# Optimization experiments

Hardware: AMD Instinct MI355X
Metric: run time of the kernel (lower is better)

## Reference

```python
import jax, jax.numpy as jnp
import numpy as np

D = 1024
H = 16
HD = D // H
EPS = 1e-5

def _layernorm(x, g, b):
    mu = jnp.mean(x, axis=-1, keepdims=True)
    var = jnp.mean(jnp.square(x - mu), axis=-1, keepdims=True)
    return (x - mu) * jax.lax.rsqrt(var + EPS) * g + b

def setup_inputs() -> dict:
    key = jax.random.key(0)
    ks = jax.random.split(key, 12)
    B, Sq, Skv = 8, 1024, 1024
    s = 1.0 / np.sqrt(D)  # xavier-ish scale
    return {
        "Q": jax.random.normal(ks[0], (B, Sq, D), jnp.float32),
        "K": jax.random.normal(ks[1], (B, Skv, D), jnp.float32),
        "key_padding_mask": jnp.ones((B, Skv), jnp.int32),
        "Wq": jax.random.normal(ks[2], (D, D), jnp.float32) * s,
        "bq": jnp.zeros((D,), jnp.float32),
        "Wk": jax.random.normal(ks[3], (D, D), jnp.float32) * s,
        "bk": jnp.zeros((D,), jnp.float32),
        "Wv": jax.random.normal(ks[4], (D, D), jnp.float32) * s,
        "bv": jnp.zeros((D,), jnp.float32),
        "Wp": jax.random.normal(ks[5], (D, D), jnp.float32) * s,
        "bp": jnp.zeros((D,), jnp.float32),
        "g0": jnp.ones((D,), jnp.float32),
        "beta0": jnp.zeros((D,), jnp.float32),
        "g1": jnp.ones((D,), jnp.float32),
        "beta1": jnp.zeros((D,), jnp.float32),
    }

def reference(Q, K, key_padding_mask, Wq, bq, Wk, bk, Wv, bv, Wp, bp, g0, beta0, g1, beta1):
    B, Sq, _ = Q.shape
    q = Q @ Wq + bq                      # [B,Sq,D]
    k = K @ Wk + bk                      # [B,Skv,D]
    v = K @ Wv + bv
    qh = q.reshape(B, Sq, H, HD).transpose(0, 2, 1, 3)   # [B,H,Sq,hd]
    kh = k.reshape(B, -1, H, HD).transpose(0, 2, 1, 3)   # [B,H,Skv,hd]
    vh = v.reshape(B, -1, H, HD).transpose(0, 2, 1, 3)
    attn = jnp.einsum('bhqd,bhkd->bhqk', qh, kh) / np.sqrt(HD)
    pad = (key_padding_mask == 0)[:, None, None, :]      # [B,1,1,Skv]
    attn = jnp.where(pad, -jnp.inf, attn)
    attn = jax.nn.softmax(attn, axis=-1)
    ctx = jnp.einsum('bhqk,bhkd->bhqd', attn, vh)        # [B,H,Sq,hd]
    ctx = ctx.transpose(0, 2, 1, 3).reshape(B, Sq, H * HD)
    o = _layernorm(q + ctx, g0, beta0)
    o = _layernorm(o + jax.nn.gelu(o @ Wp + bp, approximate=False), g1, beta1)
    return o
```

## Files before the change

### kernel.cpp

```cpp
#include <hip/hip_runtime.h>
#include <hip/hip_bf16.h>
#include <math.h>

#define DEV __device__ __forceinline__

typedef __bf16 bf16;
typedef __bf16 bf16x8 __attribute__((ext_vector_type(8)));
typedef __bf16 bf16x4 __attribute__((ext_vector_type(4)));
typedef float f32x4 __attribute__((ext_vector_type(4)));

static constexpr int BATCH = 8, S = 1024, D = 1024, H = 16, HD = 64;
static constexpr int M = BATCH * S;

static constexpr float QSCALE = 0.18033688f;

DEV f32x4 mfma16(bf16x8 a, bf16x8 b, f32x4 c) {
  return __builtin_amdgcn_mfma_f32_16x16x32_bf16(a, b, c, 0, 0, 0);
}

DEV void gload_lds16(const void* g, void* l) {
  __builtin_amdgcn_global_load_lds(
      (__attribute__((address_space(1))) void*)(g),
      (__attribute__((address_space(3))) void*)(l), 16, 0, 0);
}

DEV bf16x8 lds_read8(const void* base, int byteoff) {
  return *(const bf16x8*)((const char*)base + byteoff);
}


__global__ void cvt_bf16_kernel(const float* __restrict__ in0, bf16* __restrict__ out0,
                                const float* __restrict__ in1, bf16* __restrict__ out1, int n) {
  const float* in = blockIdx.y ? in1 : in0;
  bf16* out = blockIdx.y ? out1 : out0;
  int i = (blockIdx.x * blockDim.x + threadIdx.x) * 4;
  int stride = gridDim.x * blockDim.x * 4;
  for (; i < n; i += stride) {
    float4 v = *(const float4*)(in + i);
    bf16x4 o = { (bf16)v.x, (bf16)v.y, (bf16)v.z, (bf16)v.w };
    *(bf16x4*)(out + i) = o;
  }
}

__global__ void transpose_cvt_kernel(const float* __restrict__ w0, bf16* __restrict__ o0,
                                     const float* __restrict__ w1, bf16* __restrict__ o1,
                                     const float* __restrict__ w2, bf16* __restrict__ o2,
                                     const float* __restrict__ w3, bf16* __restrict__ o3) {
  const int z = blockIdx.z;
  const float* in = z == 0 ? w0 : z == 1 ? w1 : z == 2 ? w2 : w3;
  bf16* out = z == 0 ? o0 : z == 1 ? o1 : z == 2 ? o2 : o3;
  __shared__ float t[32][33];
  int n0 = blockIdx.x * 32, k0 = blockIdx.y * 32;
  int tx = threadIdx.x, ty = threadIdx.y;
  for (int i = 0; i < 32; i += 8)
    t[ty + i][tx] = in[(size_t)(k0 + ty + i) * D + n0 + tx];
  __syncthreads();
  for (int i = 0; i < 32; i += 8)
    out[(size_t)(n0 + ty + i) * D + k0 + tx] = (bf16)t[tx][ty + i];
}


struct GemmOut { float* f32; bf16* b16; float scale; };

template<int MODE>
DEV void gemm_body(const bf16* A, const bf16* Bt, const float* bias,
                   float* Cf, bf16* Cb, float osc,
                   bf16* As, bf16* Bs) {
  constexpr int K = 1024, N = 1024, BK = 32;
  const int tid = threadIdx.x, lane = tid & 63, wave = tid >> 6;
  int f = blockIdx.y * 8 + blockIdx.x;
  f = (f & 7) * 64 + (f >> 3);
  const int bm = f >> 3, bn = f & 7;
  const int wr = wave >> 1, wc = wave & 1;
  f32x4 acc[4][4] = {};
  const char* Ab = (const char*)(A + (size_t)bm * 128 * K);
  const char* Bb = (const char*)(Bt + (size_t)bn * 128 * K);

  for (int kt = 0; kt < K / BK; ++kt) {
    __syncthreads();
    const int k0b = kt * (BK * 2);
    for (int i = 0; i < 2; ++i) {
      int cbase = (wave * 2 + i) * 1024;
      int off = cbase + lane * 16;
      int row = off >> 6, col = off & 63;
      gload_lds16(Ab + (size_t)row * (K * 2) + k0b + col, (char*)As + cbase);
      gload_lds16(Bb + (size_t)row * (K * 2) + k0b + col, (char*)Bs + cbase);
    }
    __syncthreads();
    bf16x8 af[4], bfr[4];
    for (int mi = 0; mi < 4; ++mi)
      af[mi] = lds_read8(As, (wr * 64 + mi * 16 + (lane & 15)) * 64 + (lane >> 4) * 16);
    for (int ni = 0; ni < 4; ++ni)
      bfr[ni] = lds_read8(Bs, (wc * 64 + ni * 16 + (lane & 15)) * 64 + (lane >> 4) * 16);
    for (int mi = 0; mi < 4; ++mi)
      for (int ni = 0; ni < 4; ++ni)
        acc[mi][ni] = mfma16(af[mi], bfr[ni], acc[mi][ni]);
  }

  const int rbase = bm * 128 + wr * 64;
  const int cbase = bn * 128 + wc * 64;
  for (int ni = 0; ni < 4; ++ni) {
    int col = cbase + ni * 16 + (lane & 15);
    float bv = bias[col];
    for (int mi = 0; mi < 4; ++mi) {
      int row0 = rbase + mi * 16 + (lane >> 4) * 4;
      for (int r = 0; r < 4; ++r) {
        float v = acc[mi][ni][r] + bv;
        size_t idx = (size_t)(row0 + r) * N + col;
        if (MODE == 0) { Cf[idx] = v; Cb[idx] = (bf16)(v * osc); }
        if (MODE == 1) { Cb[idx] = (bf16)v; }
        if (MODE == 2) { Cf[idx] = v; }
      }
    }
  }
}

__global__ __launch_bounds__(256) void gemm_qkv_kernel(
    const bf16* __restrict__ Qb, const bf16* __restrict__ Kb,
    const bf16* __restrict__ Wqt, const bf16* __restrict__ Wkt, const bf16* __restrict__ Wvt,
    const float* __restrict__ bq, const float* __restrict__ bk, const float* __restrict__ bv,
    float* __restrict__ qf, bf16* __restrict__ qb,
    bf16* __restrict__ kb, bf16* __restrict__ vb)
{
  __shared__ bf16 As[128 * 32];
  __shared__ bf16 Bs[128 * 32];
  const int z = blockIdx.z;
  if (z == 0)      gemm_body<0>(Qb, Wqt, bq, qf, qb, QSCALE, As, Bs);
  else if (z == 1) gemm_body<1>(Kb, Wkt, bk, nullptr, kb, 1.f, As, Bs);
  else             gemm_body<1>(Kb, Wvt, bv, nullptr, vb, 1.f, As, Bs);
}

__global__ __launch_bounds__(256) void gemm_p_kernel(
    const bf16* __restrict__ A, const bf16* __restrict__ Bt,
    const float* __restrict__ bias, float* __restrict__ Cf)
{
  __shared__ bf16 As[128 * 32];
  __shared__ bf16 Bs[128 * 32];
  gemm_body<2>(A, Bt, bias, Cf, nullptr, 1.f, As, Bs);
}


DEV int swz(int row, int colb) { return row * 128 + (colb ^ ((row & 7) << 4)); }

__global__ __launch_bounds__(256) void attn_kernel(
    const bf16* __restrict__ q, const bf16* __restrict__ k, const bf16* __restrict__ v,
    const int* __restrict__ mask, float* __restrict__ ctx)
{
  __shared__ bf16 Kl[64 * 64];
  __shared__ bf16 Vt[64 * 64];
  __shared__ bf16 Pl[4][2][16 * 72];
  const int tid = threadIdx.x, lane = tid & 63, wave = tid >> 6;
  const int g = lane >> 4, lo = lane & 15;
  const int bh = blockIdx.y, b = bh >> 4, h = bh & 15;
  const int q0w = blockIdx.x * 128 + wave * 32;
  const size_t base = (size_t)b * S * D + (size_t)h * HD;

  bf16x8 qf[2][2];
#pragma unroll
  for (int qs = 0; qs < 2; ++qs)
#pragma unroll
    for (int c = 0; c < 2; ++c)
      qf[qs][c] = *(const bf16x8*)(q + base + (size_t)(q0w + qs * 16 + lo) * D + c * 32 + g * 8);

  f32x4 oaccT[2][4] = {};
  float mrow[2] = {-1e30f, -1e30f}, lrow[2] = {0.f, 0.f};

  for (int kt = 0; kt < S / 64; ++kt) {
    const int kv0 = kt * 64;
    __syncthreads();
#pragma unroll
    for (int rr = 0; rr < 2; ++rr) {
      int off = (rr * 256 + tid) * 16;
      int row = off >> 7, colb = off & 127;
      bf16x8 val = *(const bf16x8*)((const char*)(k + base + (size_t)(kv0 + row) * D) + colb);
      *(bf16x8*)((char*)Kl + swz(row, colb)) = val;
    }
#pragma unroll
    for (int rr = 0; rr < 2; ++rr) {
      int kvr = rr * 32 + wave * 8;
      bf16x8 val;
#pragma unroll
      for (int i = 0; i < 8; ++i)
        val[i] = v[base + (size_t)(kv0 + kvr + i) * D + lane];
      *(bf16x8*)((char*)Vt + swz(lane, kvr * 2)) = val;
    }
    __syncthreads();

    bf16x8 kf[4][2];
#pragma unroll
    for (int ct = 0; ct < 4; ++ct)
#pragma unroll
      for (int c = 0; c < 2; ++c)
        kf[ct][c] = lds_read8(Kl, swz(ct * 16 + lo, c * 64 + g * 16));

    unsigned long long mv = __ballot(mask[b * S + kv0 + lane] != 0);
    unsigned long long mq = mv >> (g * 4);

#pragma unroll
    for (int qs = 0; qs < 2; ++qs) {
      f32x4 sacc[4];
#pragma unroll
      for (int ct = 0; ct < 4; ++ct) {
        sacc[ct] = (f32x4){0.f, 0.f, 0.f, 0.f};
#pragma unroll
        for (int c = 0; c < 2; ++c)
          sacc[ct] = mfma16(kf[ct][c], qf[qs][c], sacc[ct]);
      }
      float pv[4][4];
      float mx = -1e30f;
#pragma unroll
      for (int ct = 0; ct < 4; ++ct)
#pragma unroll
        for (int r = 0; r < 4; ++r) {
          float s = sacc[ct][r];
          bool ok = (mq >> (ct * 16 + r)) & 1ull;
          s = ok ? s : -1e30f;
          pv[ct][r] = s;
          mx = fmaxf(mx, s);
        }
      mx = fmaxf(mx, __shfl_xor(mx, 16));
      mx = fmaxf(mx, __shfl_xor(mx, 32));
      if (__any(mx > mrow[qs] + 11.5f)) {
        float mnew = fmaxf(mrow[qs], mx);
        float fsc = exp2f(mrow[qs] - mnew);
        mrow[qs] = mnew;
        lrow[qs] *= fsc;
#pragma unroll
        for (int od = 0; od < 4; ++od)
          oaccT[qs][od] *= fsc;
      }
      float rs = 0.f;
      char* Pb = (char*)Pl[wave][qs];
#pragma unroll
      for (int ct = 0; ct < 4; ++ct) {
        float p0 = exp2f(pv[ct][0] - mrow[qs]);
        float p1 = exp2f(pv[ct][1] - mrow[qs]);
        float p2 = exp2f(pv[ct][2] - mrow[qs]);
        float p3 = exp2f(pv[ct][3] - mrow[qs]);
        rs += (p0 + p1) + (p2 + p3);
        bf16x4 w = { (bf16)p0, (bf16)p1, (bf16)p2, (bf16)p3 };
        *(bf16x4*)(Pb + lo * 144 + ct * 32 + g * 8) = w;
      }
      rs += __shfl_xor(rs, 16);
      rs += __shfl_xor(rs, 32);
      lrow[qs] += rs;
    }

    bf16x8 pf[2][2];
#pragma unroll
    for (int qs = 0; qs < 2; ++qs)
#pragma unroll
      for (int c = 0; c < 2; ++c)
        pf[qs][c] = lds_read8(Pl[wave][qs], lo * 144 + c * 64 + g * 16);
#pragma unroll
    for (int od = 0; od < 4; ++od) {
      bf16x8 vf0 = lds_read8(Vt, swz(od * 16 + lo, 0 * 64 + g * 16));
      bf16x8 vf1 = lds_read8(Vt, swz(od * 16 + lo, 1 * 64 + g * 16));
#pragma unroll
      for (int qs = 0; qs < 2; ++qs) {
        oaccT[qs][od] = mfma16(vf0, pf[qs][0], oaccT[qs][od]);
        oaccT[qs][od] = mfma16(vf1, pf[qs][1], oaccT[qs][od]);
      }
    }
  }

#pragma unroll
  for (int qs = 0; qs < 2; ++qs) {
    float linv = 1.0f / lrow[qs];
    size_t rowb = ((size_t)b * S + q0w + qs * 16 + lo) * D + h * HD;
#pragma unroll
    for (int od = 0; od < 4; ++od) {
      f32x4 o = oaccT[qs][od] * linv;
      *(f32x4*)(ctx + rowb + od * 16 + g * 4) = o;
    }
  }
}


DEV void block_stats(float s, float s2, float* red, int tid, float& mu, float& rstd) {
  for (int off = 32; off > 0; off >>= 1) {
    s += __shfl_down(s, off);
    s2 += __shfl_down(s2, off);
  }
  int wave = tid >> 6, lane = tid & 63;
  if (lane == 0) { red[wave] = s; red[4 + wave] = s2; }
  __syncthreads();
  float S1 = red[0] + red[1] + red[2] + red[3];
  float S2 = red[4] + red[5] + red[6] + red[7];
  mu = S1 * (1.f / 1024.f);
  rstd = rsqrtf(S2 * (1.f / 1024.f) - mu * mu + 1e-5f);
}

__global__ __launch_bounds__(256) void ln0_kernel(
    const float* __restrict__ qf, const float* __restrict__ ctx,
    const float* __restrict__ g, const float* __restrict__ beta,
    float* __restrict__ of, bf16* __restrict__ ob)
{
  __shared__ float red[8];
  const int row = blockIdx.x, tid = threadIdx.x;
  const size_t base = (size_t)row * D;
  float4 x = *(const float4*)(qf + base + tid * 4);
  float4 c = *(const float4*)(ctx + base + tid * 4);
  x.x += c.x; x.y += c.y; x.z += c.z; x.w += c.w;
  float mu, rstd;
  block_stats(x.x + x.y + x.z + x.w,
              x.x * x.x + x.y * x.y + x.z * x.z + x.w * x.w, red, tid, mu, rstd);
  float4 gv = *(const float4*)(g + tid * 4);
  float4 bv = *(const float4*)(beta + tid * 4);
  float o0 = (x.x - mu) * rstd * gv.x + bv.x;
  float o1 = (x.y - mu) * rstd * gv.y + bv.y;
  float o2 = (x.z - mu) * rstd * gv.z + bv.z;
  float o3 = (x.w - mu) * rstd * gv.w + bv.w;
  *(float4*)(of + base + tid * 4) = make_float4(o0, o1, o2, o3);
  bf16x4 o = { (bf16)o0, (bf16)o1, (bf16)o2, (bf16)o3 };
  *(bf16x4*)(ob + base + tid * 4) = o;
}

DEV float gelu_exact(float t) { return 0.5f * t * (1.f + erff(t * 0.70710678118654752f)); }

__global__ __launch_bounds__(256) void ln1_kernel(
    const float* __restrict__ of, const float* __restrict__ pf,
    const float* __restrict__ g, const float* __restrict__ beta,
    float* __restrict__ out)
{
  __shared__ float red[8];
  const int row = blockIdx.x, tid = threadIdx.x;
  const size_t base = (size_t)row * D;
  float4 x = *(const float4*)(of + base + tid * 4);
  float4 p = *(const float4*)(pf + base + tid * 4);
  x.x += gelu_exact(p.x); x.y += gelu_exact(p.y);
  x.z += gelu_exact(p.z); x.w += gelu_exact(p.w);
  float mu, rstd;
  block_stats(x.x + x.y + x.z + x.w,
              x.x * x.x + x.y * x.y + x.z * x.z + x.w * x.w, red, tid, mu, rstd);
  float4 gv = *(const float4*)(g + tid * 4);
  float4 bv = *(const float4*)(beta + tid * 4);
  float o0 = (x.x - mu) * rstd * gv.x + bv.x;
  float o1 = (x.y - mu) * rstd * gv.y + bv.y;
  float o2 = (x.z - mu) * rstd * gv.z + bv.z;
  float o3 = (x.w - mu) * rstd * gv.w + bv.w;
  *(float4*)(out + base + tid * 4) = make_float4(o0, o1, o2, o3);
}


extern "C" void kernel_launch(void* const* d_in, const int* in_sizes, int n_in,
                              void* d_out, int out_size, void* d_ws, size_t ws_size,
                              hipStream_t stream) {
  const float* Q     = (const float*)d_in[0];
  const float* K     = (const float*)d_in[1];
  const int*   mask  = (const int*)d_in[2];
  const float* Wq    = (const float*)d_in[3];
  const float* bq    = (const float*)d_in[4];
  const float* Wk    = (const float*)d_in[5];
  const float* bk    = (const float*)d_in[6];
  const float* Wv    = (const float*)d_in[7];
  const float* bv    = (const float*)d_in[8];
  const float* Wp    = (const float*)d_in[9];
  const float* bp    = (const float*)d_in[10];
  const float* g0    = (const float*)d_in[11];
  const float* beta0 = (const float*)d_in[12];
  const float* g1    = (const float*)d_in[13];
  const float* beta1 = (const float*)d_in[14];
  float* out = (float*)d_out;

  char* w = (char*)d_ws;
  const size_t MB = 1u << 20;
  bf16* Qb  = (bf16*)(w + 0 * MB);
  bf16* Kb  = (bf16*)(w + 16 * MB);
  bf16* Wqt = (bf16*)(w + 32 * MB);
  bf16* Wkt = (bf16*)(w + 34 * MB);
  bf16* Wvt = (bf16*)(w + 36 * MB);
  bf16* Wpt = (bf16*)(w + 38 * MB);
  float* qf = (float*)(w + 40 * MB);
  bf16* qb  = (bf16*)(w + 72 * MB);
  bf16* kb  = (bf16*)(w + 88 * MB);
  bf16* vb  = (bf16*)(w + 104 * MB);
  float* ctx = (float*)(w + 120 * MB);
  float* pf  = ctx;
  float* of  = (float*)(w + 152 * MB);
  bf16* ob   = (bf16*)(w + 0 * MB);

  dim3 cg(1024, 2);
  cvt_bf16_kernel<<<cg, 256, 0, stream>>>(Q, Qb, K, Kb, M * D);
  dim3 tb(32, 8), tg(32, 32, 4);
  transpose_cvt_kernel<<<tg, tb, 0, stream>>>(Wq, Wqt, Wk, Wkt, Wv, Wvt, Wp, Wpt);

  dim3 gq(8, 64, 3);
  gemm_qkv_kernel<<<gq, 256, 0, stream>>>(Qb, Kb, Wqt, Wkt, Wvt, bq, bk, bv, qf, qb, kb, vb);

  dim3 ag(S / 128, BATCH * H);
  attn_kernel<<<ag, 256, 0, stream>>>(qb, kb, vb, mask, ctx);

  ln0_kernel<<<M, 256, 0, stream>>>(qf, ctx, g0, beta0, of, ob);
  dim3 gp(8, 64);
  gemm_p_kernel<<<gp, 256, 0, stream>>>(ob, Wpt, bp, pf);
  ln1_kernel<<<M, 256, 0, stream>>>(of, pf, g1, beta1, out);
}
```

Measured before the change: 381.4 us.

## Rework attention with 32x32 MFMA, register P exchange, and double-buffered K/V

Rewrites the attention kernel to use 32x32x16 bf16 MFMA tiles (one 32-row query tile per wave) instead of 16x16 tiles. The P matrix is passed between the two MFMA stages in registers via permlane32_swap rather than through LDS. K/V tiles are double-buffered, with global loads for the next tile issued before compute, and the grid is remapped so heads group per XCD. It also adds a fast path for fully unmasked tiles, s_setprio around MFMA blocks, and an occupancy hint. These target LDS traffic, barriers, and load latency, at the cost of more register pressure and twice the LDS for K/V.

```diff
diff --git a/kernel.cpp b/kernel.cpp
--- a/kernel.cpp
+++ b/kernel.cpp
@@ -7,7 +7,12 @@
 typedef __bf16 bf16;
 typedef __bf16 bf16x8 __attribute__((ext_vector_type(8)));
 typedef __bf16 bf16x4 __attribute__((ext_vector_type(4)));
+typedef __bf16 bf16x2 __attribute__((ext_vector_type(2)));
 typedef float f32x4 __attribute__((ext_vector_type(4)));
+typedef float f32x16 __attribute__((ext_vector_type(16)));
+typedef int i32x2 __attribute__((ext_vector_type(2)));
+typedef unsigned int u32;
+typedef unsigned long long u64;
 
 static constexpr int BATCH = 8, S = 1024, D = 1024, H = 16, HD = 64;
 static constexpr int M = BATCH * S;
@@ -16,6 +21,9 @@
 
 DEV f32x4 mfma16(bf16x8 a, bf16x8 b, f32x4 c) {
   return __builtin_amdgcn_mfma_f32_16x16x32_bf16(a, b, c, 0, 0, 0);
+}
+DEV f32x16 mfma32(bf16x8 a, bf16x8 b, f32x16 c) {
+  return __builtin_amdgcn_mfma_f32_32x32x16_bf16(a, b, c, 0, 0, 0);
 }
 
 DEV void gload_lds16(const void* g, void* l) {
@@ -26,6 +34,11 @@
 
 DEV bf16x8 lds_read8(const void* base, int byteoff) {
   return *(const bf16x8*)((const char*)base + byteoff);
+}
+
+DEV u32 packbf(float a, float b) {
+  bf16x2 t = { (bf16)a, (bf16)b };
+  return __builtin_bit_cast(u32, t);
 }
 
 
@@ -60,8 +73,6 @@
 }
 
 
-struct GemmOut { float* f32; bf16* b16; float scale; };
-
 template<int MODE>
 DEV void gemm_body(const bf16* A, const bf16* Bt, const float* bias,
                    float* Cf, bf16* Cb, float osc,
@@ -142,138 +153,173 @@
 
 DEV int swz(int row, int colb) { return row * 128 + (colb ^ ((row & 7) << 4)); }
 
-__global__ __launch_bounds__(256) void attn_kernel(
+__global__ __launch_bounds__(256, 3) void attn_kernel(
     const bf16* __restrict__ q, const bf16* __restrict__ k, const bf16* __restrict__ v,
     const int* __restrict__ mask, float* __restrict__ ctx)
 {
-  __shared__ bf16 Kl[64 * 64];
-  __shared__ bf16 Vt[64 * 64];
-  __shared__ bf16 Pl[4][2][16 * 72];
+  __shared__ bf16 Kl[2][64 * 64];
+  __shared__ bf16 Vt[2][64 * 64];
   const int tid = threadIdx.x, lane = tid & 63, wave = tid >> 6;
-  const int g = lane >> 4, lo = lane & 15;
-  const int bh = blockIdx.y, b = bh >> 4, h = bh & 15;
-  const int q0w = blockIdx.x * 128 + wave * 32;
+  const int hi = lane >> 5, lq = lane & 31;
+  const int wg = blockIdx.x;
+  const int xcd = wg & 7, ix = wg >> 3;
+  const int bh = xcd * 16 + (ix & 15);
+  const int qt = ix >> 4;
+  const int b = bh >> 4, h = bh & 15;
+  const int q0 = qt * 128 + wave * 32;
   const size_t base = (size_t)b * S * D + (size_t)h * HD;
 
-  bf16x8 qf[2][2];
-#pragma unroll
-  for (int qs = 0; qs < 2; ++qs)
-#pragma unroll
-    for (int c = 0; c < 2; ++c)
-      qf[qs][c] = *(const bf16x8*)(q + base + (size_t)(q0w + qs * 16 + lo) * D + c * 32 + g * 8);
-
-  f32x4 oaccT[2][4] = {};
-  float mrow[2] = {-1e30f, -1e30f}, lrow[2] = {0.f, 0.f};
+  bf16x8 qf[4];
+#pragma unroll
+  for (int hc = 0; hc < 4; ++hc)
+    qf[hc] = *(const bf16x8*)(q + base + (size_t)(q0 + lq) * D + hc * 16 + hi * 8);
+
+  f32x16 oaccT[2] = {};
+  float mrow = -3e38f, lrow = 0.f;
+
+  bf16x8 kst[2], vst[2];
+  const int koff = tid * 16;
+  const int krow = koff >> 7, kcol = koff & 127;
+
+#define LOADK(KV0)                                                              \
+  {                                                                             \
+    _Pragma("unroll")                                                           \
+    for (int rr = 0; rr < 2; ++rr)                                              \
+      kst[rr] = *(const bf16x8*)((const char*)(k + base +                       \
+                 (size_t)((KV0) + rr * 32 + krow) * D) + kcol);                 \
+    _Pragma("unroll")                                                           \
+    for (int rr = 0; rr < 2; ++rr) {                                            \
+      int kvr = rr * 32 + wave * 8;                                             \
+      _Pragma("unroll")                                                         \
+      for (int i = 0; i < 8; ++i)                                               \
+        vst[rr][i] = v[base + (size_t)((KV0) + kvr + i) * D + lane];            \
+    }                                                                           \
+  }
+
+#define WRITEK(BI)                                                              \
+  {                                                                             \
+    _Pragma("unroll")                                                           \
+    for (int rr = 0; rr < 2; ++rr)                                              \
+      *(bf16x8*)((char*)Kl[BI] + swz(rr * 32 + krow, kcol)) = kst[rr];          \
+    _Pragma("unroll")                                                           \
+    for (int rr = 0; rr < 2; ++rr)                                              \
+      *(bf16x8*)((char*)Vt[BI] + swz(lane, (rr * 32 + wave * 8) * 2)) = vst[rr];\
+  }
+
+  LOADK(0);
+  WRITEK(0);
 
   for (int kt = 0; kt < S / 64; ++kt) {
+    const int cur = kt & 1;
     const int kv0 = kt * 64;
     __syncthreads();
-#pragma unroll
-    for (int rr = 0; rr < 2; ++rr) {
-      int off = (rr * 256 + tid) * 16;
-      int row = off >> 7, colb = off & 127;
-      bf16x8 val = *(const bf16x8*)((const char*)(k + base + (size_t)(kv0 + row) * D) + colb);
-      *(bf16x8*)((char*)Kl + swz(row, colb)) = val;
-    }
-#pragma unroll
-    for (int rr = 0; rr < 2; ++rr) {
-      int kvr = rr * 32 + wave * 8;
-      bf16x8 val;
-#pragma unroll
-      for (int i = 0; i < 8; ++i)
-        val[i] = v[base + (size_t)(kv0 + kvr + i) * D + lane];
-      *(bf16x8*)((char*)Vt + swz(lane, kvr * 2)) = val;
-    }
-    __syncthreads();
-
-    bf16x8 kf[4][2];
-#pragma unroll
-    for (int ct = 0; ct < 4; ++ct)
-#pragma unroll
-      for (int c = 0; c < 2; ++c)
-        kf[ct][c] = lds_read8(Kl, swz(ct * 16 + lo, c * 64 + g * 16));
-
-    unsigned long long mv = __ballot(mask[b * S + kv0 + lane] != 0);
-    unsigned long long mq = mv >> (g * 4);
-
-#pragma unroll
-    for (int qs = 0; qs < 2; ++qs) {
-      f32x4 sacc[4];
-#pragma unroll
-      for (int ct = 0; ct < 4; ++ct) {
-        sacc[ct] = (f32x4){0.f, 0.f, 0.f, 0.f};
-#pragma unroll
-        for (int c = 0; c < 2; ++c)
-          sacc[ct] = mfma16(kf[ct][c], qf[qs][c], sacc[ct]);
+    if (kt < S / 64 - 1) LOADK(kv0 + 64);
+
+    const char* Kb_ = (const char*)Kl[cur];
+    const char* Vb_ = (const char*)Vt[cur];
+
+    u64 mv = __ballot(mask[b * S + kv0 + lane] != 0);
+
+    f32x16 sacc[2];
+    __builtin_amdgcn_s_setprio(1);
+#pragma unroll
+    for (int sub = 0; sub < 2; ++sub) {
+      f32x16 a = {};
+#pragma unroll
+      for (int hc = 0; hc < 4; ++hc) {
+        bf16x8 kf = lds_read8(Kb_, swz(sub * 32 + lq, hc * 32 + hi * 16));
+        a = mfma32(kf, qf[hc], a);
       }
-      float pv[4][4];
-      float mx = -1e30f;
-#pragma unroll
-      for (int ct = 0; ct < 4; ++ct)
-#pragma unroll
-        for (int r = 0; r < 4; ++r) {
-          float s = sacc[ct][r];
-          bool ok = (mq >> (ct * 16 + r)) & 1ull;
-          s = ok ? s : -1e30f;
-          pv[ct][r] = s;
-          mx = fmaxf(mx, s);
+      sacc[sub] = a;
+    }
+    __builtin_amdgcn_s_setprio(0);
+
+    float mx = -3e38f;
+    if (mv == ~0ull) {
+#pragma unroll
+      for (int sub = 0; sub < 2; ++sub)
+#pragma unroll
+        for (int r = 0; r < 16; ++r) mx = fmaxf(mx, sacc[sub][r]);
+    } else {
+      u64 mqh = mv >> (hi * 4);
+#pragma unroll
+      for (int sub = 0; sub < 2; ++sub)
+#pragma unroll
+        for (int rr = 0; rr < 4; ++rr)
+#pragma unroll
+          for (int rm = 0; rm < 4; ++rm) {
+            int reg = rr * 4 + rm;
+            bool ok = (mqh >> (rm + 8 * rr + 32 * sub)) & 1ull;
+            float s = ok ? sacc[sub][reg] : -1e30f;
+            sacc[sub][reg] = s;
+            mx = fmaxf(mx, s);
+          }
+    }
+    mx = fmaxf(mx, __shfl_xor(mx, 32));
+
+    if (__any(mx > mrow + 11.5f)) {
+      float mnew = fmaxf(mrow, mx);
+      float fsc = exp2f(mrow - mnew);
+      mrow = mnew;
+      lrow *= fsc;
+      oaccT[0] *= fsc;
+      oaccT[1] *= fsc;
+    }
+
+    float rs = 0.f;
+    u32 W[2][4][2];
+#pragma unroll
+    for (int sub = 0; sub < 2; ++sub)
+#pragma unroll
+      for (int rr = 0; rr < 4; ++rr)
+#pragma unroll
+        for (int hh = 0; hh < 2; ++hh) {
+          float p0 = exp2f(sacc[sub][rr * 4 + 2 * hh] - mrow);
+          float p1 = exp2f(sacc[sub][rr * 4 + 2 * hh + 1] - mrow);
+          rs += p0 + p1;
+          W[sub][rr][hh] = packbf(p0, p1);
         }
-      mx = fmaxf(mx, __shfl_xor(mx, 16));
-      mx = fmaxf(mx, __shfl_xor(mx, 32));
-      if (__any(mx > mrow[qs] + 11.5f)) {
-        float mnew = fmaxf(mrow[qs], mx);
-        float fsc = exp2f(mrow[qs] - mnew);
-        mrow[qs] = mnew;
-        lrow[qs] *= fsc;
-#pragma unroll
-        for (int od = 0; od < 4; ++od)
-          oaccT[qs][od] *= fsc;
+    rs += __shfl_xor(rs, 32);
+    lrow += rs;
+
+    bf16x8 pfr[4];
+#pragma unroll
+    for (int t = 0; t < 4; ++t) {
+      const int sub = t >> 1, r0 = 2 * (t & 1);
+      i32x2 s0 = __builtin_amdgcn_permlane32_swap(
+          (int)W[sub][r0][0], (int)W[sub][r0 + 1][0], false, false);
+      i32x2 s1 = __builtin_amdgcn_permlane32_swap(
+          (int)W[sub][r0][1], (int)W[sub][r0 + 1][1], false, false);
+      u32 wd[4] = { (u32)s0[0], (u32)s1[0], (u32)s0[1], (u32)s1[1] };
+      pfr[t] = __builtin_bit_cast(bf16x8, wd);
+    }
+
+    __builtin_amdgcn_s_setprio(1);
+#pragma unroll
+    for (int hdsub = 0; hdsub < 2; ++hdsub) {
+      f32x16 a = oaccT[hdsub];
+#pragma unroll
+      for (int t = 0; t < 4; ++t) {
+        bf16x8 vf = lds_read8(Vb_, swz(hdsub * 32 + lq, t * 32 + hi * 16));
+        a = mfma32(vf, pfr[t], a);
       }
-      float rs = 0.f;
-      char* Pb = (char*)Pl[wave][qs];
-#pragma unroll
-      for (int ct = 0; ct < 4; ++ct) {
-        float p0 = exp2f(pv[ct][0] - mrow[qs]);
-        float p1 = exp2f(pv[ct][1] - mrow[qs]);
-        float p2 = exp2f(pv[ct][2] - mrow[qs]);
-        float p3 = exp2f(pv[ct][3] - mrow[qs]);
-        rs += (p0 + p1) + (p2 + p3);
-        bf16x4 w = { (bf16)p0, (bf16)p1, (bf16)p2, (bf16)p3 };
-        *(bf16x4*)(Pb + lo * 144 + ct * 32 + g * 8) = w;
-      }
-      rs += __shfl_xor(rs, 16);
-      rs += __shfl_xor(rs, 32);
-      lrow[qs] += rs;
-    }
-
-    bf16x8 pf[2][2];
-#pragma unroll
-    for (int qs = 0; qs < 2; ++qs)
-#pragma unroll
-      for (int c = 0; c < 2; ++c)
-        pf[qs][c] = lds_read8(Pl[wave][qs], lo * 144 + c * 64 + g * 16);
-#pragma unroll
-    for (int od = 0; od < 4; ++od) {
-      bf16x8 vf0 = lds_read8(Vt, swz(od * 16 + lo, 0 * 64 + g * 16));
-      bf16x8 vf1 = lds_read8(Vt, swz(od * 16 + lo, 1 * 64 + g * 16));
-#pragma unroll
-      for (int qs = 0; qs < 2; ++qs) {
-        oaccT[qs][od] = mfma16(vf0, pf[qs][0], oaccT[qs][od]);
-        oaccT[qs][od] = mfma16(vf1, pf[qs][1], oaccT[qs][od]);
-      }
-    }
-  }
-
-#pragma unroll
-  for (int qs = 0; qs < 2; ++qs) {
-    float linv = 1.0f / lrow[qs];
-    size_t rowb = ((size_t)b * S + q0w + qs * 16 + lo) * D + h * HD;
-#pragma unroll
-    for (int od = 0; od < 4; ++od) {
-      f32x4 o = oaccT[qs][od] * linv;
-      *(f32x4*)(ctx + rowb + od * 16 + g * 4) = o;
-    }
-  }
+      oaccT[hdsub] = a;
+    }
+    __builtin_amdgcn_s_setprio(0);
+
+    if (kt < S / 64 - 1) WRITEK(cur ^ 1);
+  }
+
+  float linv = 1.0f / lrow;
+  size_t rowb = ((size_t)b * S + q0 + lq) * D + (size_t)h * HD;
+#pragma unroll
+  for (int hdsub = 0; hdsub < 2; ++hdsub)
+#pragma unroll
+    for (int rr = 0; rr < 4; ++rr) {
+      f32x4 o = { oaccT[hdsub][rr * 4 + 0] * linv, oaccT[hdsub][rr * 4 + 1] * linv,
+                  oaccT[hdsub][rr * 4 + 2] * linv, oaccT[hdsub][rr * 4 + 3] * linv };
+      *(f32x4*)(ctx + rowb + 32 * hdsub + 8 * rr + 4 * hi) = o;
+    }
 }
 
 
@@ -388,8 +434,7 @@
   dim3 gq(8, 64, 3);
   gemm_qkv_kernel<<<gq, 256, 0, stream>>>(Qb, Kb, Wqt, Wkt, Wvt, bq, bk, bv, qf, qb, kb, vb);
 
-  dim3 ag(S / 128, BATCH * H);
-  attn_kernel<<<ag, 256, 0, stream>>>(qb, kb, vb, mask, ctx);
+  attn_kernel<<<1024, 256, 0, stream>>>(qb, kb, vb, mask, ctx);
 
   ln0_kernel<<<M, 256, 0, stream>>>(qf, ctx, g0, beta0, of, ob);
   dim3 gp(8, 64);
```

Measured after the change: 363.2 us. 1.05x faster.
